# Performance work log

Hardware: AMD Instinct MI355X
Metric: run time of the kernel (lower is better)

## Reference

```python
import jax, jax.numpy as jnp
import numpy as np

B, T, V = 32, 100, 20000
E, H, M, DD = 128, 128, 64, 2


def setup_inputs() -> dict:
    key = jax.random.key(0)
    ks = jax.random.split(key, 12)
    x = jax.random.uniform(ks[0], (B, T, V), dtype=jnp.float32)
    # zero out trailing timesteps per example so Masking layer matters
    lens = jax.random.randint(ks[1], (B,), T * 3 // 4, T + 1)
    tmask = (jnp.arange(T)[None, :] < lens[:, None]).astype(jnp.float32)
    x = x * tmask[:, :, None]
    a = jax.random.uniform(ks[2], (B, V), dtype=jnp.float32)
    d = jax.random.normal(ks[3], (B, DD), dtype=jnp.float32)
    # parameters
    emb = jax.random.uniform(ks[4], (V, E), minval=-0.1, maxval=0.1, dtype=jnp.float32)
    s = 1.0 / np.sqrt(E)
    gru_k = jax.random.uniform(ks[5], (E, 3 * H), minval=-s, maxval=s, dtype=jnp.float32)
    gru_rk = jax.random.normal(ks[6], (H, 3 * H), dtype=jnp.float32) / np.sqrt(H)
    gru_b_i = jnp.zeros((3 * H,), jnp.float32)   # input bias (reset_after=True)
    gru_b_r = jnp.zeros((3 * H,), jnp.float32)   # recurrent bias
    s1 = 1.0 / np.sqrt(H + E)
    W1 = jax.random.uniform(ks[7], (H + E, M), minval=-s1, maxval=s1, dtype=jnp.float32)
    b1 = jnp.zeros((M,), jnp.float32)
    s2 = 1.0 / np.sqrt(M + DD)
    W2 = jax.random.uniform(ks[8], (M + DD, 1), minval=-s2, maxval=s2, dtype=jnp.float32)
    b2 = jnp.zeros((1,), jnp.float32)
    return dict(x=x, a=a, d=d, emb=emb, gru_k=gru_k, gru_rk=gru_rk,
                gru_b_i=gru_b_i, gru_b_r=gru_b_r, W1=W1, b1=b1, W2=W2, b2=b2)


def _gru_final_state(xe, mask, gru_k, gru_rk, gru_b_i, gru_b_r):
    # xe: [B,T,E], mask: [B,T] bool. Keras GRU, reset_after=True, eval mode (dropout off).
    Hn = gru_rk.shape[0]
    x_proj = jnp.einsum('bte,eh->bth', xe, gru_k) + gru_b_i  # [B,T,3H]

    def step(h, inp):
        xp_t, m_t = inp                      # [B,3H], [B]
        rec = h @ gru_rk + gru_b_r           # [B,3H]
        xz, xr, xh = jnp.split(xp_t, 3, axis=-1)
        rz, rr, rh = jnp.split(rec, 3, axis=-1)
        z = jax.nn.sigmoid(xz + rz)
        r = jax.nn.sigmoid(xr + rr)
        hh = jnp.tanh(xh + r * rh)
        h_new = z * h + (1.0 - z) * hh
        h = jnp.where(m_t[:, None], h_new, h)  # masked steps carry state
        return h, None

    h0 = jnp.zeros((xe.shape[0], Hn), xe.dtype)
    h_final, _ = jax.lax.scan(step, h0, (jnp.swapaxes(x_proj, 0, 1), jnp.swapaxes(mask, 0, 1)))
    return h_final


def reference(x, a, d, emb, gru_k, gru_rk, gru_b_i, gru_b_r, W1, b1, W2, b2):
    ae = jnp.tanh(a @ emb)                       # [B,E]
    xe = jnp.tanh(jnp.einsum('btv,ve->bte', x, emb))  # [B,T,E]
    mask = jnp.any(xe != 0.0, axis=-1)           # Masking(mask_value=0.0)
    h = _gru_final_state(xe, mask, gru_k, gru_rk, gru_b_i, gru_b_r)  # [B,H]
    c = jnp.tanh(jnp.concatenate([h, ae], axis=1) @ W1 + b1)         # [B,M]
    out = jax.nn.sigmoid(jnp.concatenate([c, d], axis=1) @ W2 + b2)  # [B,1]
    return out
```

## Files before the change

### kernel.cpp

```cpp
#include <hip/hip_runtime.h>

typedef __attribute__((ext_vector_type(8))) short short8;
typedef __attribute__((ext_vector_type(4))) float float4v;

#define V_ 20000
#define KS 8
#define NT 10
#define LSTR 264

__device__ __forceinline__ unsigned short f2bf(float f) {
    union { float f; unsigned int u; } v; v.f = f;
    unsigned int u = v.u;
    u += 0x7fffu + ((u >> 16) & 1u);
    return (unsigned short)(u >> 16);
}

__device__ __forceinline__ float fast_tanh(float x) {
    float xc = fminf(15.f, fmaxf(-15.f, x));
    float e = __expf(2.f * xc);
    return (e - 1.f) / (e + 1.f);
}

__device__ __forceinline__ float sigmoidf_(float x) {
    float xc = fminf(30.f, fmaxf(-30.f, x));
    return 1.f / (1.f + __expf(-xc));
}

__global__ __launch_bounds__(256) void cvt_embT(const float* __restrict__ emb,
                                                unsigned short* __restrict__ embT) {
    __shared__ unsigned short tile[128 * 65];
    int tid = threadIdx.x;
    int k0 = blockIdx.x * 64;
    const float4v* e4 = (const float4v*)emb;
    #pragma unroll
    for (int c = 0; c < 8; ++c) {
        int l4 = c * 256 + tid;
        int k = l4 >> 5;
        int n4 = l4 & 31;
        float4v f = {0.f, 0.f, 0.f, 0.f};
        if (k0 + k < V_) f = e4[(size_t)(k0 + k) * 32 + n4];
        tile[(n4 * 4 + 0) * 65 + k] = f2bf(f.x);
        tile[(n4 * 4 + 1) * 65 + k] = f2bf(f.y);
        tile[(n4 * 4 + 2) * 65 + k] = f2bf(f.z);
        tile[(n4 * 4 + 3) * 65 + k] = f2bf(f.w);
    }
    __syncthreads();
    #pragma unroll
    for (int c = 0; c < 4; ++c) {
        int l8 = c * 256 + tid;
        int n = l8 >> 3, seg = l8 & 7;
        int kk = k0 + seg * 8;
        if (kk < V_) {
            short8 v;
            #pragma unroll
            for (int i = 0; i < 8; ++i) v[i] = (short)tile[n * 65 + seg * 8 + i];
            *(short8*)(embT + (size_t)n * V_ + kk) = v;
        }
    }
}

__global__ __launch_bounds__(256) void big_gemm(const float* __restrict__ x,
                                                const float* __restrict__ a,
                                                const unsigned short* __restrict__ embT,
                                                float* __restrict__ partial) {
    __shared__ unsigned short Alds[2][16 * LSTR];
    int tid = threadIdx.x;
    int w = tid >> 6, lane = tid & 63;
    int ln = lane & 15, quad = lane >> 4;
    int bx = blockIdx.x, by = blockIdx.y;
    int r0 = bx * 16;

    int ustart = by * 78 + (by < 1 ? by : 1);
    int nu = 78 + (by < 1 ? 1 : 0);
    int kbase = ustart * 32;
    int klen = nu * 32;

    const float* srcP[4];
    #pragma unroll
    for (int j = 0; j < 4; ++j) {
        int rg = r0 + w + 4 * j;
        const float* base = (rg < 3200) ? (x + (size_t)rg * V_)
                                        : (a + (size_t)(rg - 3200) * V_);
        srcP[j] = base + kbase + lane * 4;
    }
    const unsigned short* bp0 = embT + (size_t)((w * 2 + 0) * 16 + ln) * V_ + kbase + quad * 8;
    const unsigned short* bp1 = embT + (size_t)((w * 2 + 1) * 16 + ln) * V_ + kbase + quad * 8;

    float4v acc0 = {0.f, 0.f, 0.f, 0.f};
    float4v acc1 = {0.f, 0.f, 0.f, 0.f};
    float4v f0, f1, f2, f3;

    int wbr = w + 0;

    f0 = *(const float4v*)(srcP[0]);
    f1 = *(const float4v*)(srcP[1]);
    f2 = *(const float4v*)(srcP[2]);
    f3 = *(const float4v*)(srcP[3]);
    {
        unsigned short* dst = &Alds[0][lane * 4];
        unsigned short s[16];
        s[0]=f2bf(f0.x); s[1]=f2bf(f0.y); s[2]=f2bf(f0.z); s[3]=f2bf(f0.w);
        s[4]=f2bf(f1.x); s[5]=f2bf(f1.y); s[6]=f2bf(f1.z); s[7]=f2bf(f1.w);
        s[8]=f2bf(f2.x); s[9]=f2bf(f2.y); s[10]=f2bf(f2.z); s[11]=f2bf(f2.w);
        s[12]=f2bf(f3.x); s[13]=f2bf(f3.y); s[14]=f2bf(f3.z); s[15]=f2bf(f3.w);
        #pragma unroll
        for (int j = 0; j < 4; ++j) {
            int rr = wbr + 4 * j;
            *(uint2*)&dst[rr * LSTR] = *(uint2*)&s[j * 4];
        }
    }
    __syncthreads();

    for (int t = 0; t < NT; ++t) {
        int buf = t & 1;
        bool more = (t + 1 < NT);
        if (more) {
            int nlim = klen - (t + 1) * 256;
            bool ok = (lane * 4 < nlim);
            int off = (t + 1) * 256;
            float4v z = {0.f, 0.f, 0.f, 0.f};
            f0 = ok ? *(const float4v*)(srcP[0] + off) : z;
            f1 = ok ? *(const float4v*)(srcP[1] + off) : z;
            f2 = ok ? *(const float4v*)(srcP[2] + off) : z;
            f3 = ok ? *(const float4v*)(srcP[3] + off) : z;
        }
        const unsigned short* al = &Alds[buf][ln * LSTR + quad * 8];
        const unsigned short* b0p = bp0 + t * 256;
        const unsigned short* b1p = bp1 + t * 256;
        #pragma unroll
        for (int kk = 0; kk < 8; ++kk) {
            short8 af = *(const short8*)(al + kk * 32);
            short8 bf0 = *(const short8*)(b0p + kk * 32);
            short8 bf1 = *(const short8*)(b1p + kk * 32);
            acc0 = __builtin_amdgcn_mfma_f32_16x16x32_bf16(af, bf0, acc0, 0, 0, 0);
            acc1 = __builtin_amdgcn_mfma_f32_16x16x32_bf16(af, bf1, acc1, 0, 0, 0);
        }
        if (more) {
            unsigned short* dst = &Alds[buf ^ 1][lane * 4];
            unsigned short s[16];
            s[0]=f2bf(f0.x); s[1]=f2bf(f0.y); s[2]=f2bf(f0.z); s[3]=f2bf(f0.w);
            s[4]=f2bf(f1.x); s[5]=f2bf(f1.y); s[6]=f2bf(f1.z); s[7]=f2bf(f1.w);
            s[8]=f2bf(f2.x); s[9]=f2bf(f2.y); s[10]=f2bf(f2.z); s[11]=f2bf(f2.w);
            s[12]=f2bf(f3.x); s[13]=f2bf(f3.y); s[14]=f2bf(f3.z); s[15]=f2bf(f3.w);
            #pragma unroll
            for (int j = 0; j < 4; ++j) {
                int rr = wbr + 4 * j;
                *(uint2*)&dst[rr * LSTR] = *(uint2*)&s[j * 4];
            }
        }
        __syncthreads();
    }

    float* dst = partial + ((size_t)by * 3232 + r0 + quad * 4) * 128 + ln;
    #pragma unroll
    for (int reg = 0; reg < 4; ++reg) {
        dst[(size_t)reg * 128 + (w * 2 + 0) * 16] = acc0[reg];
        dst[(size_t)reg * 128 + (w * 2 + 1) * 16] = acc1[reg];
    }
}

__global__ __launch_bounds__(128) void reduce_tanh(const float* __restrict__ partial,
                                                   float* __restrict__ xe,
                                                   float* __restrict__ ae,
                                                   float* __restrict__ maskg) {
    int row = blockIdx.x;
    int e = threadIdx.x;
    float s = 0.f;
    #pragma unroll
    for (int k = 0; k < KS; ++k)
        s += partial[((size_t)k * 3232 + row) * 128 + e];
    float v = fast_tanh(s);
    if (row < 3200) {
        xe[(size_t)row * 128 + e] = v;
        __shared__ int any;
        if (e == 0) any = 0;
        __syncthreads();
        if (v != 0.f) any = 1;
        __syncthreads();
        if (e == 0) maskg[row] = any ? 1.f : 0.f;
    } else {
        ae[(row - 3200) * 128 + e] = v;
    }
}

__global__ __launch_bounds__(384) void xproj_kernel(const float* __restrict__ xe,
                                                    const float* __restrict__ gru_k,
                                                    const float* __restrict__ b_i,
                                                    float* __restrict__ xproj) {
    __shared__ float xs[16 * 128];
    int tid = threadIdx.x;
    int row0 = blockIdx.x * 16;
    const float4v* src = (const float4v*)(xe + (size_t)row0 * 128);
    float4v* dstl = (float4v*)xs;
    #pragma unroll
    for (int c = 0; c < 2; ++c) {
        int i4 = c * 384 + tid;
        if (i4 < 512) dstl[i4] = src[i4];
    }
    __syncthreads();
    int j = tid;
    float acc[16];
    #pragma unroll
    for (int r = 0; r < 16; ++r) acc[r] = 0.f;
    float bi = b_i[j];
    for (int k4 = 0; k4 < 32; ++k4) {
        float g0 = gru_k[(k4 * 4 + 0) * 384 + j];
        float g1 = gru_k[(k4 * 4 + 1) * 384 + j];
        float g2 = gru_k[(k4 * 4 + 2) * 384 + j];
        float g3 = gru_k[(k4 * 4 + 3) * 384 + j];
        #pragma unroll
        for (int r = 0; r < 16; ++r) {
            float4v xv = *(const float4v*)&xs[r * 128 + k4 * 4];
            acc[r] = fmaf(xv.x, g0, acc[r]);
            acc[r] = fmaf(xv.y, g1, acc[r]);
            acc[r] = fmaf(xv.z, g2, acc[r]);
            acc[r] = fmaf(xv.w, g3, acc[r]);
        }
    }
    #pragma unroll
    for (int r = 0; r < 16; ++r)
        xproj[(size_t)(row0 + r) * 384 + j] = acc[r] + bi;
}

__global__ __launch_bounds__(384) void gru_kernel(const float* __restrict__ xproj,
                                                  const float* __restrict__ maskg,
                                                  const float* __restrict__ gru_rk,
                                                  const float* __restrict__ b_r,
                                                  float* __restrict__ hout) {
    int b = blockIdx.x;
    int j = threadIdx.x;
    float w[128];
    #pragma unroll
    for (int k = 0; k < 128; ++k) w[k] = gru_rk[k * 384 + j];
    float br = b_r[j];
    __shared__ float4v hs4[32];
    __shared__ float recs[384];
    float* hs = (float*)hs4;
    float hreg = 0.f;
    if (j < 128) hs[j] = 0.f;
    const float* xp_base = xproj + (size_t)b * 100 * 384;
    const float* mk = maskg + b * 100;
    float xz = 0.f, xr = 0.f, xh = 0.f;
    if (j < 128) { xz = xp_base[j]; xr = xp_base[128 + j]; xh = xp_base[256 + j]; }
    __syncthreads();
    for (int t = 0; t < 100; ++t) {
        float nxz = 0.f, nxr = 0.f, nxh = 0.f;
        if (t < 99 && j < 128) {
            const float* nb = xp_base + (t + 1) * 384;
            nxz = nb[j]; nxr = nb[128 + j]; nxh = nb[256 + j];
        }
        float s0 = 0.f, s1 = 0.f, s2 = 0.f, s3 = 0.f;
        #pragma unroll
        for (int k4 = 0; k4 < 32; ++k4) {
            float4v hv = hs4[k4];
            s0 = fmaf(hv.x, w[k4 * 4 + 0], s0);
            s1 = fmaf(hv.y, w[k4 * 4 + 1], s1);
            s2 = fmaf(hv.z, w[k4 * 4 + 2], s2);
            s3 = fmaf(hv.w, w[k4 * 4 + 3], s3);
        }
        recs[j] = br + ((s0 + s1) + (s2 + s3));
        __syncthreads();
        if (j < 128) {
            float z = sigmoidf_(xz + recs[j]);
            float r = sigmoidf_(xr + recs[128 + j]);
            float hh = fast_tanh(xh + r * recs[256 + j]);
            float hn = z * hreg + (1.f - z) * hh;
            hreg = (mk[t] != 0.f) ? hn : hreg;
            hs[j] = hreg;
        }
        __syncthreads();
        xz = nxz; xr = nxr; xh = nxh;
    }
    if (j < 128) hout[b * 128 + j] = hreg;
}

__global__ __launch_bounds__(64) void head_kernel(const float* __restrict__ hout,
                                                  const float* __restrict__ ae,
                                                  const float* __restrict__ d,
                                                  const float* __restrict__ W1,
                                                  const float* __restrict__ b1,
                                                  const float* __restrict__ W2,
                                                  const float* __restrict__ b2,
                                                  float* __restrict__ out) {
    int b = blockIdx.x;
    int m = threadIdx.x;
    float s = b1[m];
    const float* hb = hout + b * 128;
    const float* ab = ae + b * 128;
    #pragma unroll 4
    for (int k = 0; k < 128; ++k) s = fmaf(hb[k], W1[k * 64 + m], s);
    #pragma unroll 4
    for (int k = 0; k < 128; ++k) s = fmaf(ab[k], W1[(128 + k) * 64 + m], s);
    float c = fast_tanh(s);
    float p = c * W2[m];
    #pragma unroll
    for (int off = 32; off > 0; off >>= 1) p += __shfl_down(p, off);
    if (m == 0) {
        p += d[b * 2 + 0] * W2[64] + d[b * 2 + 1] * W2[65] + b2[0];
        out[b] = sigmoidf_(p);
    }
}

extern "C" void kernel_launch(void* const* d_in, const int* in_sizes, int n_in,
                              void* d_out, int out_size, void* d_ws, size_t ws_size,
                              hipStream_t stream) {
    (void)in_sizes; (void)n_in; (void)out_size; (void)ws_size;
    const float* x      = (const float*)d_in[0];
    const float* a      = (const float*)d_in[1];
    const float* d      = (const float*)d_in[2];
    const float* emb    = (const float*)d_in[3];
    const float* gru_k  = (const float*)d_in[4];
    const float* gru_rk = (const float*)d_in[5];
    const float* gbi    = (const float*)d_in[6];
    const float* gbr    = (const float*)d_in[7];
    const float* W1     = (const float*)d_in[8];
    const float* b1     = (const float*)d_in[9];
    const float* W2     = (const float*)d_in[10];
    const float* b2     = (const float*)d_in[11];
    float* out = (float*)d_out;

    char* ws = (char*)d_ws;
    unsigned short* embT = (unsigned short*)(ws);
    float* xe      = (float*)(ws + 5120000);
    float* ae      = (float*)(ws + 6758400);
    float* maskg   = (float*)(ws + 6774784);
    float* xproj   = (float*)(ws + 6787584);
    float* hout    = (float*)(ws + 11702784);
    float* partial = (float*)(ws + 11719168);

    hipLaunchKernelGGL(cvt_embT,    dim3(313),      dim3(256), 0, stream, emb, embT);
    hipLaunchKernelGGL(big_gemm,    dim3(202, KS),  dim3(256), 0, stream, x, a, embT, partial);
    hipLaunchKernelGGL(reduce_tanh, dim3(3232),     dim3(128), 0, stream, partial, xe, ae, maskg);
    hipLaunchKernelGGL(xproj_kernel,dim3(200),      dim3(384), 0, stream, xe, gru_k, gbi, xproj);
    hipLaunchKernelGGL(gru_kernel,  dim3(32),       dim3(384), 0, stream, xproj, maskg, gru_rk, gbr, hout);
    hipLaunchKernelGGL(head_kernel, dim3(32),       dim3(64),  0, stream, hout, ae, d, W1, b1, W2, b2, out);
}
```

Baseline: 597.4 us.

## Pre-convert activations to padded bf16 buffer before the embedding GEMM

```diff
diff --git a/kernel.cpp b/kernel.cpp
--- a/kernel.cpp
+++ b/kernel.cpp
@@ -4,6 +4,7 @@
 typedef __attribute__((ext_vector_type(4))) float float4v;
 
 #define V_ 20000
+#define VP 20480
 #define KS 8
 #define NT 10
 #define LSTR 264
@@ -24,6 +25,32 @@
 __device__ __forceinline__ float sigmoidf_(float x) {
     float xc = fminf(30.f, fmaxf(-30.f, x));
     return 1.f / (1.f + __expf(-xc));
+}
+
+__global__ __launch_bounds__(320) void cvt_xb(const float* __restrict__ x,
+                                              const float* __restrict__ a,
+                                              unsigned short* __restrict__ xb) {
+    int bx = blockIdx.x;
+    int row = bx >> 1, half = bx & 1;
+    int t = threadIdx.x;
+    const float* __restrict__ src = (row < 3200) ? (x + (size_t)row * V_)
+                                                 : (a + (size_t)(row - 3200) * V_);
+    unsigned short* __restrict__ dst = xb + (size_t)row * VP + half * 10240;
+    #pragma unroll
+    for (int i = 0; i < 4; ++i) {
+        int s = (t + i * 320) * 8;
+        int gs = half * 10240 + s;
+        short8 v;
+        if (gs < V_) {
+            float4v f0 = *(const float4v*)(src + gs);
+            float4v f1 = *(const float4v*)(src + gs + 4);
+            v[0]=(short)f2bf(f0.x); v[1]=(short)f2bf(f0.y); v[2]=(short)f2bf(f0.z); v[3]=(short)f2bf(f0.w);
+            v[4]=(short)f2bf(f1.x); v[5]=(short)f2bf(f1.y); v[6]=(short)f2bf(f1.z); v[7]=(short)f2bf(f1.w);
+        } else {
+            v = (short8){0,0,0,0,0,0,0,0};
+        }
+        *(short8*)(dst + s) = v;
+    }
 }
 
 __global__ __launch_bounds__(256) void cvt_embT(const float* __restrict__ emb,
@@ -50,17 +77,14 @@
         int l8 = c * 256 + tid;
         int n = l8 >> 3, seg = l8 & 7;
         int kk = k0 + seg * 8;
-        if (kk < V_) {
-            short8 v;
-            #pragma unroll
-            for (int i = 0; i < 8; ++i) v[i] = (short)tile[n * 65 + seg * 8 + i];
-            *(short8*)(embT + (size_t)n * V_ + kk) = v;
-        }
-    }
-}
-
-__global__ __launch_bounds__(256) void big_gemm(const float* __restrict__ x,
-                                                const float* __restrict__ a,
+        short8 v;
+        #pragma unroll
+        for (int i = 0; i < 8; ++i) v[i] = (short)tile[n * 65 + seg * 8 + i];
+        *(short8*)(embT + (size_t)n * VP + kk) = v;
+    }
+}
+
+__global__ __launch_bounds__(256) void big_gemm(const unsigned short* __restrict__ xb,
                                                 const unsigned short* __restrict__ embT,
                                                 float* __restrict__ partial) {
     __shared__ unsigned short Alds[2][16 * LSTR];
@@ -69,60 +93,29 @@
     int ln = lane & 15, quad = lane >> 4;
     int bx = blockIdx.x, by = blockIdx.y;
     int r0 = bx * 16;
-
-    int ustart = by * 78 + (by < 1 ? by : 1);
-    int nu = 78 + (by < 1 ? 1 : 0);
-    int kbase = ustart * 32;
-    int klen = nu * 32;
-
-    const float* srcP[4];
-    #pragma unroll
-    for (int j = 0; j < 4; ++j) {
-        int rg = r0 + w + 4 * j;
-        const float* base = (rg < 3200) ? (x + (size_t)rg * V_)
-                                        : (a + (size_t)(rg - 3200) * V_);
-        srcP[j] = base + kbase + lane * 4;
-    }
-    const unsigned short* bp0 = embT + (size_t)((w * 2 + 0) * 16 + ln) * V_ + kbase + quad * 8;
-    const unsigned short* bp1 = embT + (size_t)((w * 2 + 1) * 16 + ln) * V_ + kbase + quad * 8;
+    int kbase = by * 2560;
+
+    int sr = tid >> 4, sc = (tid & 15) * 8;
+    const unsigned short* srcA = xb + (size_t)(r0 + sr) * VP + kbase + sc;
+    const unsigned short* bp0 = embT + (size_t)((w * 2 + 0) * 16 + ln) * VP + kbase + quad * 8;
+    const unsigned short* bp1 = embT + (size_t)((w * 2 + 1) * 16 + ln) * VP + kbase + quad * 8;
 
     float4v acc0 = {0.f, 0.f, 0.f, 0.f};
     float4v acc1 = {0.f, 0.f, 0.f, 0.f};
-    float4v f0, f1, f2, f3;
-
-    int wbr = w + 0;
-
-    f0 = *(const float4v*)(srcP[0]);
-    f1 = *(const float4v*)(srcP[1]);
-    f2 = *(const float4v*)(srcP[2]);
-    f3 = *(const float4v*)(srcP[3]);
-    {
-        unsigned short* dst = &Alds[0][lane * 4];
-        unsigned short s[16];
-        s[0]=f2bf(f0.x); s[1]=f2bf(f0.y); s[2]=f2bf(f0.z); s[3]=f2bf(f0.w);
-        s[4]=f2bf(f1.x); s[5]=f2bf(f1.y); s[6]=f2bf(f1.z); s[7]=f2bf(f1.w);
-        s[8]=f2bf(f2.x); s[9]=f2bf(f2.y); s[10]=f2bf(f2.z); s[11]=f2bf(f2.w);
-        s[12]=f2bf(f3.x); s[13]=f2bf(f3.y); s[14]=f2bf(f3.z); s[15]=f2bf(f3.w);
-        #pragma unroll
-        for (int j = 0; j < 4; ++j) {
-            int rr = wbr + 4 * j;
-            *(uint2*)&dst[rr * LSTR] = *(uint2*)&s[j * 4];
-        }
-    }
+    short8 pf0, pf1;
+
+    pf0 = *(const short8*)(srcA);
+    pf1 = *(const short8*)(srcA + 128);
+    *(short8*)&Alds[0][sr * LSTR + sc]       = pf0;
+    *(short8*)&Alds[0][sr * LSTR + sc + 128] = pf1;
     __syncthreads();
 
     for (int t = 0; t < NT; ++t) {
         int buf = t & 1;
         bool more = (t + 1 < NT);
         if (more) {
-            int nlim = klen - (t + 1) * 256;
-            bool ok = (lane * 4 < nlim);
-            int off = (t + 1) * 256;
-            float4v z = {0.f, 0.f, 0.f, 0.f};
-            f0 = ok ? *(const float4v*)(srcP[0] + off) : z;
-            f1 = ok ? *(const float4v*)(srcP[1] + off) : z;
-            f2 = ok ? *(const float4v*)(srcP[2] + off) : z;
-            f3 = ok ? *(const float4v*)(srcP[3] + off) : z;
+            pf0 = *(const short8*)(srcA + (t + 1) * 256);
+            pf1 = *(const short8*)(srcA + (t + 1) * 256 + 128);
         }
         const unsigned short* al = &Alds[buf][ln * LSTR + quad * 8];
         const unsigned short* b0p = bp0 + t * 256;
@@ -136,17 +129,9 @@
             acc1 = __builtin_amdgcn_mfma_f32_16x16x32_bf16(af, bf1, acc1, 0, 0, 0);
         }
         if (more) {
-            unsigned short* dst = &Alds[buf ^ 1][lane * 4];
-            unsigned short s[16];
-            s[0]=f2bf(f0.x); s[1]=f2bf(f0.y); s[2]=f2bf(f0.z); s[3]=f2bf(f0.w);
-            s[4]=f2bf(f1.x); s[5]=f2bf(f1.y); s[6]=f2bf(f1.z); s[7]=f2bf(f1.w);
-            s[8]=f2bf(f2.x); s[9]=f2bf(f2.y); s[10]=f2bf(f2.z); s[11]=f2bf(f2.w);
-            s[12]=f2bf(f3.x); s[13]=f2bf(f3.y); s[14]=f2bf(f3.z); s[15]=f2bf(f3.w);
-            #pragma unroll
-            for (int j = 0; j < 4; ++j) {
-                int rr = wbr + 4 * j;
-                *(uint2*)&dst[rr * LSTR] = *(uint2*)&s[j * 4];
-            }
+            int nxt = buf ^ 1;
+            *(short8*)&Alds[nxt][sr * LSTR + sc]       = pf0;
+            *(short8*)&Alds[nxt][sr * LSTR + sc + 128] = pf1;
         }
         __syncthreads();
     }
@@ -321,15 +306,17 @@
 
     char* ws = (char*)d_ws;
     unsigned short* embT = (unsigned short*)(ws);
-    float* xe      = (float*)(ws + 5120000);
-    float* ae      = (float*)(ws + 6758400);
-    float* maskg   = (float*)(ws + 6774784);
-    float* xproj   = (float*)(ws + 6787584);
-    float* hout    = (float*)(ws + 11702784);
-    float* partial = (float*)(ws + 11719168);
-
-    hipLaunchKernelGGL(cvt_embT,    dim3(313),      dim3(256), 0, stream, emb, embT);
-    hipLaunchKernelGGL(big_gemm,    dim3(202, KS),  dim3(256), 0, stream, x, a, embT, partial);
+    unsigned short* xb   = (unsigned short*)(ws + 5242880);
+    float* xe      = (float*)(ws + 137625600);
+    float* ae      = (float*)(ws + 139264000);
+    float* maskg   = (float*)(ws + 139280384);
+    float* xproj   = (float*)(ws + 139293184);
+    float* hout    = (float*)(ws + 144208384);
+    float* partial = (float*)(ws + 144224768);
+
+    hipLaunchKernelGGL(cvt_xb,      dim3(6464),     dim3(320), 0, stream, x, a, xb);
+    hipLaunchKernelGGL(cvt_embT,    dim3(320),      dim3(256), 0, stream, emb, embT);
+    hipLaunchKernelGGL(big_gemm,    dim3(202, KS),  dim3(256), 0, stream, xb, embT, partial);
     hipLaunchKernelGGL(reduce_tanh, dim3(3232),     dim3(128), 0, stream, partial, xe, ae, maskg);
     hipLaunchKernelGGL(xproj_kernel,dim3(200),      dim3(384), 0, stream, xe, gru_k, gbi, xproj);
     hipLaunchKernelGGL(gru_kernel,  dim3(32),       dim3(384), 0, stream, xproj, maskg, gru_rk, gbr, hout);
```

Result: slower. 683.3 us (+14.4%).
